# Optimization experiments

Measured on AMD Instinct MI355X. Metric: run time of the kernel, lower is better.

## Reference

```python
import jax, jax.numpy as jnp
import numpy as np

HEADS = 32
K_TOP = 512  # top-k tokens gathered from KV


def conv3d(x, w, b=None, pad=0, groups=1):
    # x: [B,C,D,H,W], w: [O, I/groups, kd,kh,kw]
    out = jax.lax.conv_general_dilated(
        x, w, window_strides=(1, 1, 1), padding=[(pad, pad)] * 3,
        dimension_numbers=("NCDHW", "OIDHW", "NCDHW"), feature_group_count=groups)
    if b is not None:
        out = out + b[None, :, None, None, None]
    return out


def setup_inputs() -> dict:
    key = jax.random.key(0)
    ks = jax.random.split(key, 10)
    B, C, D, H, W = 2, 256, 16, 16, 16
    p = lambda i, shape: (jax.random.normal(ks[i], shape, jnp.float32) * 0.02)
    return {
        "x_kv": jax.random.normal(ks[0], (B, C, D, H, W), jnp.float32),
        "x_q": jax.random.normal(ks[1], (B, C, D, H, W), jnp.float32),
        "w_spa": p(2, (1, 2, 7, 7, 7)),            # SpatialAttention conv, no bias
        "w_kv": p(3, (C, 2 * C)), "b_kv": jnp.zeros((2 * C,), jnp.float32),
        "w_q": p(4, (C, C)), "b_q": jnp.zeros((C,), jnp.float32),
        "w_proj": p(5, (C, C)), "b_proj": jnp.zeros((C,), jnp.float32),
        "w_dw": p(6, (C, 1, 3, 3, 3)), "b_dw": jnp.zeros((C,), jnp.float32),  # depthwise 3x3x3
        "w_pw": p(7, (C, C, 1, 1, 1)), "b_pw": jnp.zeros((C,), jnp.float32),  # pointwise 1x1x1
    }


def reference(x_kv, x_q, w_spa, w_kv, b_kv, w_q, b_q, w_proj, b_proj,
              w_dw, b_dw, w_pw, b_pw):
    B, C, D, H, W = x_kv.shape
    N = D * H * W
    hd = C // HEADS
    scale = hd ** -0.5

    # SpatialAttention: channel mean/max -> conv(2->1, k=7, pad=3) -> sigmoid
    avg = jnp.mean(x_kv, axis=1, keepdims=True)
    mx = jnp.max(x_kv, axis=1, keepdims=True)
    spa = jax.nn.sigmoid(conv3d(jnp.concatenate([avg, mx], axis=1), w_spa, None, pad=3))
    scores = spa.reshape(B, N)                      # [B, N]
    _, idx = jax.lax.top_k(scores, K_TOP)           # [B, K] (descending, like torch.topk)

    # Full K/V projection over all N tokens (as in original), then gather top-k
    xkv_t = x_kv.reshape(B, C, N).transpose(0, 2, 1)        # [B, N, C]
    kv = xkv_t @ w_kv + b_kv                                 # [B, N, 2C]
    k_full, v_full = kv[..., :C], kv[..., C:]
    k_g = jnp.take_along_axis(k_full, idx[:, :, None], axis=1)  # [B, K, C]
    v_g = jnp.take_along_axis(v_full, idx[:, :, None], axis=1)
    k_g = k_g.reshape(B, K_TOP, HEADS, hd).transpose(0, 2, 1, 3)  # [B, h, K, d]
    v_g = v_g.reshape(B, K_TOP, HEADS, hd).transpose(0, 2, 1, 3)

    # Queries over all Nq tokens
    xq_t = x_q.reshape(B, C, N).transpose(0, 2, 1)           # [B, N, C]
    q = (xq_t @ w_q + b_q).reshape(B, N, HEADS, hd).transpose(0, 2, 1, 3)  # [B, h, N, d]

    attn = jax.nn.softmax(jnp.einsum('bhnd,bhkd->bhnk', q, k_g) * scale, axis=-1)
    out = jnp.einsum('bhnk,bhkd->bhnd', attn, v_g)           # [B, h, N, d]
    out = out.transpose(0, 2, 1, 3).reshape(B, N, C)
    out = out @ w_proj + b_proj
    out = out.transpose(0, 2, 1).reshape(B, C, D, H, W)

    # DWconv residual on full (ungathered) V
    v_vol = v_full.transpose(0, 2, 1).reshape(B, C, D, H, W)
    res = conv3d(conv3d(v_vol, w_dw, b_dw, pad=1, groups=C), w_pw, b_pw)
    return out + res
```

## Files before the change

### kernel.cpp

```cpp
#include <hip/hip_runtime.h>
#include <hip/hip_bf16.h>

typedef short bf16x8 __attribute__((ext_vector_type(8)));
typedef float f32x4 __attribute__((ext_vector_type(4)));

constexpr int CN = 256, NV = 4096, KTOP = 512;

static __device__ __forceinline__ unsigned short f2bf(float f) {
  __hip_bfloat16 h = __float2bfloat16(f);
  return *(unsigned short*)&h;
}
static __device__ __forceinline__ unsigned pack2(float a, float b) {
  return (unsigned)f2bf(a) | ((unsigned)f2bf(b) << 16);
}
static __device__ __forceinline__ float bf2f(unsigned short u) {
  return __uint_as_float(((unsigned)u) << 16);
}
static __device__ __forceinline__ unsigned packtrunc(float a, float b) {
  return (__float_as_uint(a) >> 16) | (__float_as_uint(b) & 0xFFFF0000u);
}

__global__ void __launch_bounds__(256) k_stage1(const float* __restrict__ xkv,
                                                const float* __restrict__ xq,
                                                const float* __restrict__ wkv,
                                                const float* __restrict__ wq,
                                                const float* __restrict__ wproj,
                                                const float* __restrict__ wpw,
                                                unsigned short* __restrict__ xkv_t,
                                                unsigned short* __restrict__ xq_t,
                                                float* __restrict__ avgmx,
                                                unsigned short* __restrict__ wv_t,
                                                unsigned short* __restrict__ wq_t,
                                                unsigned short* __restrict__ wcat,
                                                unsigned short* __restrict__ wk_t) {
  __shared__ float tile[64 * 68];
  int z = blockIdx.z;
  int t = threadIdx.x;
  if (z == 4) {
    __shared__ float4 ssum4[256], smax4[256];
    int blk = blockIdx.y * 64 + blockIdx.x;
    if (blk >= 64) return;
    int b = blk >> 5, n0r = (blk & 31) * 128;
    int cg = t >> 5, nl = t & 31;
    int n = n0r + nl * 4;
    const float* p = xkv + (size_t)b * CN * NV + (size_t)cg * 32 * NV + n;
    float4 s4 = make_float4(0.f, 0.f, 0.f, 0.f);
    float4 m4 = make_float4(-1e30f, -1e30f, -1e30f, -1e30f);
    for (int i = 0; i < 32; ++i) {
      float4 v = *(const float4*)&p[(size_t)i * NV];
      s4.x += v.x; s4.y += v.y; s4.z += v.z; s4.w += v.w;
      m4.x = fmaxf(m4.x, v.x); m4.y = fmaxf(m4.y, v.y);
      m4.z = fmaxf(m4.z, v.z); m4.w = fmaxf(m4.w, v.w);
    }
    ssum4[t] = s4; smax4[t] = m4;
    __syncthreads();
    if (cg == 0) {
      for (int g = 1; g < 8; ++g) {
        float4 o = ssum4[g * 32 + nl], x = smax4[g * 32 + nl];
        s4.x += o.x; s4.y += o.y; s4.z += o.z; s4.w += o.w;
        m4.x = fmaxf(m4.x, x.x); m4.y = fmaxf(m4.y, x.y);
        m4.z = fmaxf(m4.z, x.z); m4.w = fmaxf(m4.w, x.w);
      }
      float4 a4 = make_float4(s4.x * (1.0f / 256.0f), s4.y * (1.0f / 256.0f),
                              s4.z * (1.0f / 256.0f), s4.w * (1.0f / 256.0f));
      *(float4*)&avgmx[(size_t)(b * 2 + 0) * NV + n] = a4;
      *(float4*)&avgmx[(size_t)(b * 2 + 1) * NV + n] = m4;
    }
    return;
  }
  if (z >= 5) {
    if (blockIdx.x >= 4 || blockIdx.y >= 4) return;
    int role = z - 5;
    int j0 = blockIdx.x * 64, c0 = blockIdx.y * 64;
    if (role == 3) {
      int j = t >> 2, part = t & 3;
      const float* s = &wpw[(size_t)(j0 + j) * 256 + c0 + part * 16];
      unsigned w[8];
#pragma unroll
      for (int k = 0; k < 8; ++k) w[k] = pack2(s[2 * k], s[2 * k + 1]);
      uint4* p = (uint4*)&wcat[(size_t)(j0 + j) * 512 + 256 + c0 + part * 16];
      p[0] = make_uint4(w[0], w[1], w[2], w[3]);
      p[1] = make_uint4(w[4], w[5], w[6], w[7]);
      return;
    }
    const float* src; int srcLD, srcOff; unsigned short* dst; int dstLD;
    if (role == 0)      { src = wkv;   srcLD = 512; srcOff = 256; dst = wv_t; dstLD = 256; }
    else if (role == 1) { src = wq;    srcLD = 256; srcOff = 0;   dst = wq_t; dstLD = 256; }
    else if (role == 4) { src = wkv;   srcLD = 512; srcOff = 0;   dst = wk_t; dstLD = 256; }
    else                { src = wproj; srcLD = 256; srcOff = 0;   dst = wcat; dstLD = 512; }
    for (int i = 0; i < 16; ++i) {
      int id = i * 256 + t, c = id >> 6, j = id & 63;
      tile[c * 65 + j] = src[(size_t)(c0 + c) * srcLD + srcOff + j0 + j];
    }
    __syncthreads();
    int j = t & 63, part = t >> 6;
    unsigned w[8];
#pragma unroll
    for (int k = 0; k < 8; ++k)
      w[k] = pack2(tile[(part * 16 + 2 * k) * 65 + j], tile[(part * 16 + 2 * k + 1) * 65 + j]);
    uint4* p = (uint4*)&dst[(size_t)(j0 + j) * dstLD + c0 + part * 16];
    p[0] = make_uint4(w[0], w[1], w[2], w[3]);
    p[1] = make_uint4(w[4], w[5], w[6], w[7]);
    return;
  }
  int b = z & 1;
  const float* s = (z < 2 ? xkv : xq) + (size_t)b * CN * NV;
  unsigned short* d = (z < 2 ? xkv_t : xq_t) + (size_t)b * NV * 256;
  int c0 = blockIdx.y * 64, n0 = blockIdx.x * 64;
#pragma unroll
  for (int i = 0; i < 4; ++i) {
    int id = i * 256 + t, c = id >> 4, nq = (id & 15) * 4;
    *(float4*)&tile[c * 68 + nq] = *(const float4*)&s[(size_t)(c0 + c) * NV + n0 + nq];
  }
  __syncthreads();
  int n = t & 63, part = t >> 6;
  unsigned w[8];
#pragma unroll
  for (int k = 0; k < 8; ++k)
    w[k] = pack2(tile[(part * 16 + 2 * k) * 68 + n], tile[(part * 16 + 2 * k + 1) * 68 + n]);
  uint4* p = (uint4*)&d[(size_t)(n0 + n) * 256 + c0 + part * 16];
  p[0] = make_uint4(w[0], w[1], w[2], w[3]);
  p[1] = make_uint4(w[4], w[5], w[6], w[7]);
}

__global__ void __launch_bounds__(256) k_stage2(const unsigned short* __restrict__ xkv_t,
                                                const unsigned short* __restrict__ xq_t,
                                                const unsigned short* __restrict__ wv_t,
                                                const unsigned short* __restrict__ wq_t,
                                                const unsigned short* __restrict__ wk_t,
                                                const float* __restrict__ bkv,
                                                const float* __restrict__ bq,
                                                const float* __restrict__ avgmx,
                                                const float* __restrict__ wspa,
                                                unsigned short* __restrict__ v_nc,
                                                unsigned short* __restrict__ qh,
                                                unsigned short* __restrict__ k_nc,
                                                float* __restrict__ scores) {
  __shared__ alignas(16) char smem[35520];
  int z = blockIdx.z;
  int t = threadIdx.x;
  if (z == 6) {
    int id = blockIdx.y * 32 + blockIdx.x;
    if (id >= 64) return;
    float* vol = (float*)smem;
    float* ws = (float*)(smem + 32768);
    int b = id >> 5, chunk = id & 31;
    for (int i = t; i < 8192; i += 256) vol[i] = avgmx[b * 8192 + i];
    for (int i = t; i < 686; i += 256) ws[i] = wspa[i];
    __syncthreads();
    int ci = t & 1;
    int n = chunk * 128 + (t >> 1);
    int d = n >> 8, h = (n >> 4) & 15, w = n & 15;
    const float* vb = vol + ci * 4096;
    const float* wb = ws + ci * 343;
    float acc = 0.f;
    for (int kd = 0; kd < 7; ++kd) {
      int zd = d - 3 + kd; if ((unsigned)zd >= 16u) continue;
      for (int kh = 0; kh < 7; ++kh) {
        int zh = h - 3 + kh; if ((unsigned)zh >= 16u) continue;
        const float* row = vb + zd * 256 + zh * 16;
        const float* wr = wb + kd * 49 + kh * 7;
#pragma unroll
        for (int kw = 0; kw < 7; ++kw) {
          int zw = w - 3 + kw;
          if ((unsigned)zw < 16u) acc += row[zw] * wr[kw];
        }
      }
    }
    acc += __shfl_xor(acc, 1);
    if (ci == 0) scores[b * NV + n] = 1.0f / (1.0f + expf(-acc));
    return;
  }
  const float kscale = 0.35355339059327373f * 1.4426950408889634f;
  unsigned short* Als = (unsigned short*)smem;
  unsigned short* Bls = Als + 64 * 40;
  int b = z & 1, kind = z >> 1;
  const unsigned short* A = kind == 0 ? wv_t : (kind == 1 ? wq_t : wk_t);
  const unsigned short* B = (kind == 1 ? xq_t : xkv_t) + (size_t)b * NV * 256;
  const float* bias = kind == 0 ? (bkv + 256) : (kind == 1 ? bq : bkv);
  float scl = (kind == 1) ? kscale : 1.0f;
  int n0 = blockIdx.x * 128, j0 = blockIdx.y * 64;
  int wave = t >> 6, lane = t & 63;
  int l15 = lane & 15, q = lane >> 4, q8 = q * 8;
  int wj = (wave >> 1) * 32, wn = (wave & 1) * 64;
  f32x4 acc[2][4] = {};
  int arA = t >> 2, ahA = t & 3;
  int brB = t >> 1, bhB = t & 1;
  for (int c0 = 0; c0 < 256; c0 += 32) {
    __syncthreads();
    *(uint4*)&Als[arA * 40 + ahA * 8] =
        *(const uint4*)&A[(size_t)(j0 + arA) * 256 + c0 + ahA * 8];
    const unsigned short* sb = &B[(size_t)(n0 + brB) * 256 + c0 + bhB * 16];
    *(uint4*)&Bls[brB * 40 + bhB * 16]     = *(const uint4*)&sb[0];
    *(uint4*)&Bls[brB * 40 + bhB * 16 + 8] = *(const uint4*)&sb[8];
    __syncthreads();
    bf16x8 af[2], bf[4];
#pragma unroll
    for (int mt = 0; mt < 2; ++mt)
      af[mt] = *(const bf16x8*)&Als[(wj + mt * 16 + l15) * 40 + q8];
#pragma unroll
    for (int nt = 0; nt < 4; ++nt)
      bf[nt] = *(const bf16x8*)&Bls[(wn + nt * 16 + l15) * 40 + q8];
#pragma unroll
    for (int mt = 0; mt < 2; ++mt)
#pragma unroll
      for (int nt = 0; nt < 4; ++nt)
        acc[mt][nt] = __builtin_amdgcn_mfma_f32_16x16x32_bf16(af[mt], bf[nt], acc[mt][nt], 0, 0, 0);
  }
#pragma unroll
  for (int mt = 0; mt < 2; ++mt) {
    int jb = j0 + wj + mt * 16 + q * 4;
    float4 b4 = *(const float4*)&bias[jb];
#pragma unroll
    for (int nt = 0; nt < 4; ++nt) {
      int n = n0 + wn + nt * 16 + l15;
      float v0 = (acc[mt][nt][0] + b4.x) * scl;
      float v1 = (acc[mt][nt][1] + b4.y) * scl;
      float v2 = (acc[mt][nt][2] + b4.z) * scl;
      float v3 = (acc[mt][nt][3] + b4.w) * scl;
      uint2 pk = make_uint2(pack2(v0, v1), pack2(v2, v3));
      if (kind == 1) {
        int h = jb >> 3, d0 = jb & 7;
        *(uint2*)&qh[((size_t)(b * 32 + h) * NV + n) * 8 + d0] = pk;
      } else if (kind == 0) {
        *(uint2*)&v_nc[((size_t)b * NV + n) * 256 + jb] = pk;
      } else {
        *(uint2*)&k_nc[((size_t)b * NV + n) * 256 + jb] = pk;
      }
    }
  }
}

__global__ void __launch_bounds__(1024) k_stage3(const float* __restrict__ scores,
                                                 int* __restrict__ idx,
                                                 const unsigned short* __restrict__ v_nc,
                                                 const float* __restrict__ wdw,
                                                 const float* __restrict__ bdw,
                                                 unsigned short* __restrict__ aoydw) {
  int b = blockIdx.z;
  int bx = blockIdx.x;
  int tid = threadIdx.x;
  if (bx == 256) {
    __shared__ unsigned sv[4096];
    __shared__ int sB;
    __shared__ unsigned sSub, scnt;
    __shared__ unsigned hist[256];
    __shared__ int wsum[16];
    for (int t = tid; t < 4096; t += 1024) sv[t] = __float_as_uint(scores[b * NV + t]);
    if (tid == 0) scnt = 0;
    unsigned prefix = 0;
    int r = 512;
    for (int shift = 24; shift >= 0; shift -= 8) {
      if (tid < 256) hist[tid] = 0;
      __syncthreads();
      unsigned maskhi = (shift == 24) ? 0u : (0xFFFFFFFFu << (shift + 8));
      for (int i = 0; i < 4; ++i) {
        unsigned v = sv[tid + i * 1024];
        if ((v & maskhi) == prefix) atomicAdd(&hist[(v >> shift) & 255], 1u);
      }
      __syncthreads();
      if (tid < 64) {
        int lane = tid;
        unsigned h0 = hist[lane * 4 + 0], h1 = hist[lane * 4 + 1];
        unsigned h2 = hist[lane * 4 + 2], h3 = hist[lane * 4 + 3];
        unsigned s = h0 + h1 + h2 + h3;
        for (int off = 1; off < 64; off <<= 1) {
          unsigned y = __shfl_down(s, off);
          if (lane + off < 64) s += y;
        }
        unsigned tail = __shfl_down(s, 1);
        if (lane == 63) tail = 0;
        unsigned s3 = tail + h3, s2 = s3 + h2, s1 = s2 + h1, s0 = s1 + h0;
        unsigned sx[5] = {s0, s1, s2, s3, tail};
#pragma unroll
        for (int i = 0; i < 4; ++i)
          if (sx[i] >= (unsigned)r && sx[i + 1] < (unsigned)r) { sB = lane * 4 + i; sSub = sx[i + 1]; }
      }
      __syncthreads();
      prefix |= ((unsigned)sB) << shift;
      r -= (int)sSub;
      __syncthreads();
    }
    unsigned vstar = prefix;
    for (int i = 0; i < 4; ++i) {
      int t = tid * 4 + i;
      if (sv[t] > vstar) { unsigned p = atomicAdd(&scnt, 1u); idx[b * KTOP + p] = t; }
    }
    __syncthreads();
    int base = (int)scnt;
    int loc = 0;
    for (int i = 0; i < 4; ++i) loc += (sv[tid * 4 + i] == vstar);
    int lane = tid & 63, w = tid >> 6;
    int x = loc;
    for (int off = 1; off < 64; off <<= 1) {
      int y = __shfl_up(x, off);
      if (lane >= off) x += y;
    }
    if (lane == 63) wsum[w] = x;
    __syncthreads();
    int wbase = 0;
    for (int i = 0; i < w; ++i) wbase += wsum[i];
    int excl = wbase + x - loc;
    for (int i = 0; i < 4; ++i) {
      int t = tid * 4 + i;
      if (sv[t] == vstar) {
        if (excl < r) idx[b * KTOP + base + excl] = t;
        ++excl;
      }
    }
    return;
  }
  int c = tid & 255;
  float wr[27];
#pragma unroll
  for (int i = 0; i < 27; ++i) wr[i] = wdw[c * 27 + i];
  float bias = bdw[c];
  const unsigned short* src = v_nc + (size_t)b * NV * 256 + c;
  unsigned short* dst = aoydw + (size_t)b * NV * 512 + 256 + c;
  int n = bx * 16 + (tid >> 8) * 4;
  int d = n >> 8, h = (n >> 4) & 15, w = n & 15;
  float a0 = bias, a1 = bias, a2 = bias, a3 = bias;
#pragma unroll
  for (int kd = 0; kd < 3; ++kd) {
    int zd = d - 1 + kd; bool okd = (unsigned)zd < 16u;
#pragma unroll
    for (int kh = 0; kh < 3; ++kh) {
      int zh = h - 1 + kh; bool okh = okd && ((unsigned)zh < 16u);
      int rowb = zd * 256 + zh * 16;
      float v[6];
#pragma unroll
      for (int i = 0; i < 6; ++i) {
        int zw = w - 1 + i;
        bool ok = okh && ((unsigned)zw < 16u);
        v[i] = ok ? bf2f(src[(size_t)(rowb + zw) * 256]) : 0.f;
      }
      const float* wp = &wr[kd * 9 + kh * 3];
      a0 = fmaf(v[0], wp[0], fmaf(v[1], wp[1], fmaf(v[2], wp[2], a0)));
      a1 = fmaf(v[1], wp[0], fmaf(v[2], wp[1], fmaf(v[3], wp[2], a1)));
      a2 = fmaf(v[2], wp[0], fmaf(v[3], wp[1], fmaf(v[4], wp[2], a2)));
      a3 = fmaf(v[3], wp[0], fmaf(v[4], wp[1], fmaf(v[5], wp[2], a3)));
    }
  }
  dst[(size_t)(n + 0) * 512] = f2bf(a0);
  dst[(size_t)(n + 1) * 512] = f2bf(a1);
  dst[(size_t)(n + 2) * 512] = f2bf(a2);
  dst[(size_t)(n + 3) * 512] = f2bf(a3);
}

__global__ void __launch_bounds__(256) k_fattn(const unsigned short* __restrict__ qh,
                                               const unsigned short* __restrict__ k_nc,
                                               const unsigned short* __restrict__ v_nc,
                                               const int* __restrict__ idx,
                                               unsigned short* __restrict__ aoydw) {
  __shared__ int idx_l[512];
  __shared__ unsigned short vt_l[16 * 520];
  int bh = blockIdx.x;
  int b = bh >> 5, h = bh & 31;
  int t = threadIdx.x, wave = t >> 6, lane = t & 63;
  int l15 = lane & 15, quad = lane >> 4;
  const int* ib = idx + b * KTOP;
  for (int i = t; i < 512; i += 256) idx_l[i] = ib[i];
  for (int i = t; i < 512; i += 256) vt_l[8 * 520 + i] = 0x3F80;
  for (int i = t; i < 7 * 520; i += 256) vt_l[9 * 520 + i] = 0;
  for (int kk = t; kk < 512; kk += 256) {
    uint4 v = *(const uint4*)&v_nc[((size_t)b * NV + ib[kk]) * 256 + h * 8];
    unsigned short tmp[8];
    *(uint4*)tmp = v;
    int kc = kk >> 5, ka = kk & 31;
    int s = (ka < 16) ? ((ka >> 2) * 8 + (ka & 3))
                      : (((ka - 16) >> 2) * 8 + (ka & 3) + 4);
    int col = kc * 32 + s;
#pragma unroll
    for (int d = 0; d < 8; ++d) vt_l[d * 520 + col] = tmp[d];
  }
  int n0 = blockIdx.y * 128 + wave * 32;
  bf16x8 q0 = {}, q1 = {};
  if (quad == 0) {
    q0 = *(const bf16x8*)&qh[((size_t)bh * NV + n0 + l15) * 8];
    q1 = *(const bf16x8*)&qh[((size_t)bh * NV + n0 + 16 + l15) * 8];
  }
  __syncthreads();
  const unsigned short* kbase = k_nc + (size_t)b * NV * 256 + h * 8;
  f32x4 acc0 = {0.f, 0.f, 0.f, 0.f}, acc1 = {0.f, 0.f, 0.f, 0.f};
  bf16x8 kA0 = {}, kA1 = {};
  if (quad == 0) {
    kA0 = *(const bf16x8*)&kbase[(size_t)idx_l[l15] * 256];
    kA1 = *(const bf16x8*)&kbase[(size_t)idx_l[16 + l15] * 256];
  }
  for (int kc = 0; kc < 16; ++kc) {
    bf16x8 nA0 = {}, nA1 = {};
    if (quad == 0 && kc < 15) {
      nA0 = *(const bf16x8*)&kbase[(size_t)idx_l[kc * 32 + 32 + l15] * 256];
      nA1 = *(const bf16x8*)&kbase[(size_t)idx_l[kc * 32 + 48 + l15] * 256];
    }
    bf16x8 bV = *(const bf16x8*)&vt_l[l15 * 520 + kc * 32 + quad * 8];
    f32x4 z = {0.f, 0.f, 0.f, 0.f};
    f32x4 s00 = __builtin_amdgcn_mfma_f32_16x16x32_bf16(kA0, q0, z, 0, 0, 0);
    f32x4 s01 = __builtin_amdgcn_mfma_f32_16x16x32_bf16(kA1, q0, z, 0, 0, 0);
    f32x4 s10 = __builtin_amdgcn_mfma_f32_16x16x32_bf16(kA0, q1, z, 0, 0, 0);
    f32x4 s11 = __builtin_amdgcn_mfma_f32_16x16x32_bf16(kA1, q1, z, 0, 0, 0);
    uint4 P0, P1;
    P0.x = packtrunc(__builtin_amdgcn_exp2f(s00[0]), __builtin_amdgcn_exp2f(s00[1]));
    P0.y = packtrunc(__builtin_amdgcn_exp2f(s00[2]), __builtin_amdgcn_exp2f(s00[3]));
    P0.z = packtrunc(__builtin_amdgcn_exp2f(s01[0]), __builtin_amdgcn_exp2f(s01[1]));
    P0.w = packtrunc(__builtin_amdgcn_exp2f(s01[2]), __builtin_amdgcn_exp2f(s01[3]));
    P1.x = packtrunc(__builtin_amdgcn_exp2f(s10[0]), __builtin_amdgcn_exp2f(s10[1]));
    P1.y = packtrunc(__builtin_amdgcn_exp2f(s10[2]), __builtin_amdgcn_exp2f(s10[3]));
    P1.z = packtrunc(__builtin_amdgcn_exp2f(s11[0]), __builtin_amdgcn_exp2f(s11[1]));
    P1.w = packtrunc(__builtin_amdgcn_exp2f(s11[2]), __builtin_amdgcn_exp2f(s11[3]));
    acc0 = __builtin_amdgcn_mfma_f32_16x16x32_bf16(*(bf16x8*)&P0, bV, acc0, 0, 0, 0);
    acc1 = __builtin_amdgcn_mfma_f32_16x16x32_bf16(*(bf16x8*)&P1, bV, acc1, 0, 0, 0);
    kA0 = nA0; kA1 = nA1;
  }
#pragma unroll
  for (int tq = 0; tq < 2; ++tq) {
    f32x4 a = tq ? acc1 : acc0;
#pragma unroll
    for (int r = 0; r < 4; ++r) {
      float se = __shfl(a[r], quad * 16 + 8);
      float o = a[r] * (1.0f / se);
      if (l15 < 8) {
        int n = n0 + tq * 16 + quad * 4 + r;
        aoydw[((size_t)b * NV + n) * 512 + h * 8 + l15] = f2bf(o);
      }
    }
  }
}

__global__ void __launch_bounds__(256) k_final(const unsigned short* __restrict__ aoydw,
                                               const unsigned short* __restrict__ wcat,
                                               const float* __restrict__ bproj,
                                               const float* __restrict__ bpw,
                                               float* __restrict__ out) {
  __shared__ unsigned short Als[64 * 72];
  __shared__ unsigned short Bls[64 * 72];
  int n0 = blockIdx.x * 64, j0 = blockIdx.y * 64, b = blockIdx.z;
  int t = threadIdx.x;
  int wave = t >> 6, lane = t & 63;
  int l15 = lane & 15, q = lane >> 4, q8 = q * 8;
  int wn = (wave & 1) * 32, wjj = (wave >> 1) * 32;
  f32x4 acc[2][2] = {};
  const unsigned short* Abase = aoydw + (size_t)b * NV * 512;
  int ar = t >> 2, aq = t & 3;
  for (int c0 = 0; c0 < 512; c0 += 64) {
    __syncthreads();
    *(uint4*)&Als[ar * 72 + aq * 8] =
        *(const uint4*)&Abase[(size_t)(n0 + ar) * 512 + c0 + aq * 8];
    *(uint4*)&Als[ar * 72 + 32 + aq * 8] =
        *(const uint4*)&Abase[(size_t)(n0 + ar) * 512 + c0 + 32 + aq * 8];
    *(uint4*)&Bls[ar * 72 + aq * 8] =
        *(const uint4*)&wcat[(size_t)(j0 + ar) * 512 + c0 + aq * 8];
    *(uint4*)&Bls[ar * 72 + 32 + aq * 8] =
        *(const uint4*)&wcat[(size_t)(j0 + ar) * 512 + c0 + 32 + aq * 8];
    __syncthreads();
#pragma unroll
    for (int kk = 0; kk < 2; ++kk) {
      bf16x8 af[2], bf[2];
#pragma unroll
      for (int mt = 0; mt < 2; ++mt)
        af[mt] = *(const bf16x8*)&Als[(wn + mt * 16 + l15) * 72 + kk * 32 + q8];
#pragma unroll
      for (int nt = 0; nt < 2; ++nt)
        bf[nt] = *(const bf16x8*)&Bls[(wjj + nt * 16 + l15) * 72 + kk * 32 + q8];
#pragma unroll
      for (int mt = 0; mt < 2; ++mt)
#pragma unroll
        for (int nt = 0; nt < 2; ++nt)
          acc[mt][nt] = __builtin_amdgcn_mfma_f32_16x16x32_bf16(af[mt], bf[nt], acc[mt][nt], 0, 0, 0);
    }
  }
#pragma unroll
  for (int nt = 0; nt < 2; ++nt) {
    int j = j0 + wjj + nt * 16 + l15;
    float bl = bproj[j] + bpw[j];
#pragma unroll
    for (int mt = 0; mt < 2; ++mt) {
      int n = n0 + wn + mt * 16 + q * 4;
      float4 r = make_float4(acc[mt][nt][0] + bl, acc[mt][nt][1] + bl,
                             acc[mt][nt][2] + bl, acc[mt][nt][3] + bl);
      *(float4*)&out[(size_t)(b * 256 + j) * NV + n] = r;
    }
  }
}

extern "C" void kernel_launch(void* const* d_in, const int* in_sizes, int n_in,
                              void* d_out, int out_size, void* d_ws, size_t ws_size,
                              hipStream_t stream) {
  const float* x_kv   = (const float*)d_in[0];
  const float* x_q    = (const float*)d_in[1];
  const float* w_spa  = (const float*)d_in[2];
  const float* w_kv   = (const float*)d_in[3];
  const float* b_kv   = (const float*)d_in[4];
  const float* w_q    = (const float*)d_in[5];
  const float* b_q    = (const float*)d_in[6];
  const float* w_proj = (const float*)d_in[7];
  const float* b_proj = (const float*)d_in[8];
  const float* w_dw   = (const float*)d_in[9];
  const float* b_dw   = (const float*)d_in[10];
  const float* w_pw   = (const float*)d_in[11];
  const float* b_pw   = (const float*)d_in[12];
  float* out = (float*)d_out;

  const size_t MB = 1024 * 1024;
  char* ws = (char*)d_ws;
  unsigned short* xkv_t = (unsigned short*)(ws);
  unsigned short* xq_t  = (unsigned short*)(ws + 4 * MB);
  unsigned short* v_nc  = (unsigned short*)(ws + 8 * MB);
  unsigned short* qh    = (unsigned short*)(ws + 12 * MB);
  unsigned short* aoydw = (unsigned short*)(ws + 16 * MB);
  unsigned short* k_nc  = (unsigned short*)(ws + 24 * MB);
  unsigned short* wv_t  = (unsigned short*)(ws + 28 * MB);
  unsigned short* wq_t  = (unsigned short*)(ws + 28 * MB + 131072);
  unsigned short* wcat  = (unsigned short*)(ws + 28 * MB + 262144);
  unsigned short* wk_t  = (unsigned short*)(ws + 28 * MB + 524288);
  float*          avgmx = (float*)(ws + 29 * MB);
  float*          scores= (float*)(ws + 29 * MB + 65536);
  int*            idx   = (int*)  (ws + 29 * MB + 98304);

  k_stage1<<<dim3(64, 4, 10), 256, 0, stream>>>(x_kv, x_q, w_kv, w_q, w_proj, w_pw,
                                                xkv_t, xq_t, avgmx, wv_t, wq_t, wcat, wk_t);
  k_stage2<<<dim3(32, 4, 7), 256, 0, stream>>>(xkv_t, xq_t, wv_t, wq_t, wk_t, b_kv, b_q,
                                               avgmx, w_spa, v_nc, qh, k_nc, scores);
  k_stage3<<<dim3(257, 1, 2), 1024, 0, stream>>>(scores, idx, v_nc, w_dw, b_dw, aoydw);
  k_fattn<<<dim3(64, 32), 256, 0, stream>>>(qh, k_nc, v_nc, idx, aoydw);
  k_final<<<dim3(64, 4, 2), 256, 0, stream>>>(aoydw, wcat, b_proj, b_pw, out);
}
```

Before: 178.0 us.

## Fuse K and V projection GEMMs to share loaded input tiles

Stage 2 now computes the K and V projections in one block, loading each xkv_t tile into shared memory once and using it for two sets of MFMA accumulators. This halves the activation reads for the KV projection and removes the per-kind branching, at the cost of more registers and fewer blocks (grid z drops from 7 to 5). The weight transpose in stage 1 also switches to float4 loads with a padded stride of 68, and packtrunc now uses a byte permute instruction.

```diff
diff --git a/kernel.cpp b/kernel.cpp
--- a/kernel.cpp
+++ b/kernel.cpp
@@ -17,7 +17,7 @@
   return __uint_as_float(((unsigned)u) << 16);
 }
 static __device__ __forceinline__ unsigned packtrunc(float a, float b) {
-  return (__float_as_uint(a) >> 16) | (__float_as_uint(b) & 0xFFFF0000u);
+  return __builtin_amdgcn_perm(__float_as_uint(b), __float_as_uint(a), 0x07060302u);
 }
 
 __global__ void __launch_bounds__(256) k_stage1(const float* __restrict__ xkv,
@@ -88,16 +88,18 @@
     else if (role == 1) { src = wq;    srcLD = 256; srcOff = 0;   dst = wq_t; dstLD = 256; }
     else if (role == 4) { src = wkv;   srcLD = 512; srcOff = 0;   dst = wk_t; dstLD = 256; }
     else                { src = wproj; srcLD = 256; srcOff = 0;   dst = wcat; dstLD = 512; }
-    for (int i = 0; i < 16; ++i) {
-      int id = i * 256 + t, c = id >> 6, j = id & 63;
-      tile[c * 65 + j] = src[(size_t)(c0 + c) * srcLD + srcOff + j0 + j];
+#pragma unroll
+    for (int i = 0; i < 4; ++i) {
+      int id = i * 256 + t, c = id >> 4, j4 = (id & 15) * 4;
+      *(float4*)&tile[c * 68 + j4] =
+          *(const float4*)&src[(size_t)(c0 + c) * srcLD + srcOff + j0 + j4];
     }
     __syncthreads();
     int j = t & 63, part = t >> 6;
     unsigned w[8];
 #pragma unroll
     for (int k = 0; k < 8; ++k)
-      w[k] = pack2(tile[(part * 16 + 2 * k) * 65 + j], tile[(part * 16 + 2 * k + 1) * 65 + j]);
+      w[k] = pack2(tile[(part * 16 + 2 * k) * 68 + j], tile[(part * 16 + 2 * k + 1) * 68 + j]);
     uint4* p = (uint4*)&dst[(size_t)(j0 + j) * dstLD + c0 + part * 16];
     p[0] = make_uint4(w[0], w[1], w[2], w[3]);
     p[1] = make_uint4(w[4], w[5], w[6], w[7]);
@@ -139,7 +141,7 @@
   __shared__ alignas(16) char smem[35520];
   int z = blockIdx.z;
   int t = threadIdx.x;
-  if (z == 6) {
+  if (z == 4) {
     int id = blockIdx.y * 32 + blockIdx.x;
     if (id >= 64) return;
     float* vol = (float*)smem;
@@ -172,24 +174,73 @@
     return;
   }
   const float kscale = 0.35355339059327373f * 1.4426950408889634f;
-  unsigned short* Als = (unsigned short*)smem;
-  unsigned short* Bls = Als + 64 * 40;
-  int b = z & 1, kind = z >> 1;
-  const unsigned short* A = kind == 0 ? wv_t : (kind == 1 ? wq_t : wk_t);
-  const unsigned short* B = (kind == 1 ? xq_t : xkv_t) + (size_t)b * NV * 256;
-  const float* bias = kind == 0 ? (bkv + 256) : (kind == 1 ? bq : bkv);
-  float scl = (kind == 1) ? kscale : 1.0f;
-  int n0 = blockIdx.x * 128, j0 = blockIdx.y * 64;
   int wave = t >> 6, lane = t & 63;
   int l15 = lane & 15, q = lane >> 4, q8 = q * 8;
   int wj = (wave >> 1) * 32, wn = (wave & 1) * 64;
-  f32x4 acc[2][4] = {};
+  int n0 = blockIdx.x * 128, j0 = blockIdx.y * 64;
   int arA = t >> 2, ahA = t & 3;
   int brB = t >> 1, bhB = t & 1;
+  if (z < 2) {
+    int b = z;
+    unsigned short* Avls = (unsigned short*)smem;
+    unsigned short* Akls = Avls + 64 * 40;
+    unsigned short* Bls  = Akls + 64 * 40;
+    const unsigned short* B = xkv_t + (size_t)b * NV * 256;
+    f32x4 accv[2][4] = {}, acck[2][4] = {};
+    for (int c0 = 0; c0 < 256; c0 += 32) {
+      __syncthreads();
+      *(uint4*)&Avls[arA * 40 + ahA * 8] =
+          *(const uint4*)&wv_t[(size_t)(j0 + arA) * 256 + c0 + ahA * 8];
+      *(uint4*)&Akls[arA * 40 + ahA * 8] =
+          *(const uint4*)&wk_t[(size_t)(j0 + arA) * 256 + c0 + ahA * 8];
+      const unsigned short* sb = &B[(size_t)(n0 + brB) * 256 + c0 + bhB * 16];
+      *(uint4*)&Bls[brB * 40 + bhB * 16]     = *(const uint4*)&sb[0];
+      *(uint4*)&Bls[brB * 40 + bhB * 16 + 8] = *(const uint4*)&sb[8];
+      __syncthreads();
+      bf16x8 afv[2], afk[2], bf[4];
+#pragma unroll
+      for (int mt = 0; mt < 2; ++mt) {
+        afv[mt] = *(const bf16x8*)&Avls[(wj + mt * 16 + l15) * 40 + q8];
+        afk[mt] = *(const bf16x8*)&Akls[(wj + mt * 16 + l15) * 40 + q8];
+      }
+#pragma unroll
+      for (int nt = 0; nt < 4; ++nt)
+        bf[nt] = *(const bf16x8*)&Bls[(wn + nt * 16 + l15) * 40 + q8];
+#pragma unroll
+      for (int mt = 0; mt < 2; ++mt)
+#pragma unroll
+        for (int nt = 0; nt < 4; ++nt) {
+          accv[mt][nt] = __builtin_amdgcn_mfma_f32_16x16x32_bf16(afv[mt], bf[nt], accv[mt][nt], 0, 0, 0);
+          acck[mt][nt] = __builtin_amdgcn_mfma_f32_16x16x32_bf16(afk[mt], bf[nt], acck[mt][nt], 0, 0, 0);
+        }
+    }
+#pragma unroll
+    for (int mt = 0; mt < 2; ++mt) {
+      int jb = j0 + wj + mt * 16 + q * 4;
+      float4 bv = *(const float4*)&bkv[256 + jb];
+      float4 bk = *(const float4*)&bkv[jb];
+#pragma unroll
+      for (int nt = 0; nt < 4; ++nt) {
+        int n = n0 + wn + nt * 16 + l15;
+        *(uint2*)&v_nc[((size_t)b * NV + n) * 256 + jb] =
+            make_uint2(pack2(accv[mt][nt][0] + bv.x, accv[mt][nt][1] + bv.y),
+                       pack2(accv[mt][nt][2] + bv.z, accv[mt][nt][3] + bv.w));
+        *(uint2*)&k_nc[((size_t)b * NV + n) * 256 + jb] =
+            make_uint2(pack2(acck[mt][nt][0] + bk.x, acck[mt][nt][1] + bk.y),
+                       pack2(acck[mt][nt][2] + bk.z, acck[mt][nt][3] + bk.w));
+      }
+    }
+    return;
+  }
+  int b = z - 2;
+  unsigned short* Als = (unsigned short*)smem;
+  unsigned short* Bls = Als + 64 * 40;
+  const unsigned short* B = xq_t + (size_t)b * NV * 256;
+  f32x4 acc[2][4] = {};
   for (int c0 = 0; c0 < 256; c0 += 32) {
     __syncthreads();
     *(uint4*)&Als[arA * 40 + ahA * 8] =
-        *(const uint4*)&A[(size_t)(j0 + arA) * 256 + c0 + ahA * 8];
+        *(const uint4*)&wq_t[(size_t)(j0 + arA) * 256 + c0 + ahA * 8];
     const unsigned short* sb = &B[(size_t)(n0 + brB) * 256 + c0 + bhB * 16];
     *(uint4*)&Bls[brB * 40 + bhB * 16]     = *(const uint4*)&sb[0];
     *(uint4*)&Bls[brB * 40 + bhB * 16 + 8] = *(const uint4*)&sb[8];
@@ -210,23 +261,14 @@
 #pragma unroll
   for (int mt = 0; mt < 2; ++mt) {
     int jb = j0 + wj + mt * 16 + q * 4;
-    float4 b4 = *(const float4*)&bias[jb];
+    float4 b4 = *(const float4*)&bq[jb];
+    int h = jb >> 3, d0 = jb & 7;
 #pragma unroll
     for (int nt = 0; nt < 4; ++nt) {
       int n = n0 + wn + nt * 16 + l15;
-      float v0 = (acc[mt][nt][0] + b4.x) * scl;
-      float v1 = (acc[mt][nt][1] + b4.y) * scl;
-      float v2 = (acc[mt][nt][2] + b4.z) * scl;
-      float v3 = (acc[mt][nt][3] + b4.w) * scl;
-      uint2 pk = make_uint2(pack2(v0, v1), pack2(v2, v3));
-      if (kind == 1) {
-        int h = jb >> 3, d0 = jb & 7;
-        *(uint2*)&qh[((size_t)(b * 32 + h) * NV + n) * 8 + d0] = pk;
-      } else if (kind == 0) {
-        *(uint2*)&v_nc[((size_t)b * NV + n) * 256 + jb] = pk;
-      } else {
-        *(uint2*)&k_nc[((size_t)b * NV + n) * 256 + jb] = pk;
-      }
+      *(uint2*)&qh[((size_t)(b * 32 + h) * NV + n) * 8 + d0] =
+          make_uint2(pack2((acc[mt][nt][0] + b4.x) * kscale, (acc[mt][nt][1] + b4.y) * kscale),
+                     pack2((acc[mt][nt][2] + b4.z) * kscale, (acc[mt][nt][3] + b4.w) * kscale));
     }
   }
 }
@@ -519,7 +561,7 @@
 
   k_stage1<<<dim3(64, 4, 10), 256, 0, stream>>>(x_kv, x_q, w_kv, w_q, w_proj, w_pw,
                                                 xkv_t, xq_t, avgmx, wv_t, wq_t, wcat, wk_t);
-  k_stage2<<<dim3(32, 4, 7), 256, 0, stream>>>(xkv_t, xq_t, wv_t, wq_t, wk_t, b_kv, b_q,
+  k_stage2<<<dim3(32, 4, 5), 256, 0, stream>>>(xkv_t, xq_t, wv_t, wq_t, wk_t, b_kv, b_q,
                                                avgmx, w_spa, v_nc, qh, k_nc, scores);
   k_stage3<<<dim3(257, 1, 2), 1024, 0, stream>>>(scores, idx, v_nc, w_dw, b_dw, aoydw);
   k_fattn<<<dim3(64, 32), 256, 0, stream>>>(qh, k_nc, v_nc, idx, aoydw);
```

Result: no change. 178.3 us (+0.2%).
